# Performance work log

Hardware: AMD Instinct MI355X
Metric: run time of the kernel (lower is better)

## Reference

```python
import jax, jax.numpy as jnp
import numpy as np

B, S, P, E, H, FF = 4, 16, 256, 768, 12, 3072
HD = E // H
LN_EPS = 1e-5


def _layernorm(x, g, b):
    m = jnp.mean(x, axis=-1, keepdims=True)
    v = jnp.mean((x - m) ** 2, axis=-1, keepdims=True)
    return (x - m) * jax.lax.rsqrt(v + LN_EPS) * g + b


def _qkv(x, wqkv, bqkv):
    # wqkv: [3, E, E] (in, out layout), bqkv: [3, E]
    qkv = jnp.einsum('bspe,tef->tbspf', x, wqkv) + bqkv[:, None, None, None, :]
    q, k, v = qkv
    b, s, p, e = x.shape
    shp = (b, s, p, H, HD)
    return q.reshape(shp), k.reshape(shp), v.reshape(shp)


def spatial_attn(x, wqkv, bqkv, wo, bo, g, beta):
    q, k, v = _qkv(x, wqkv, bqkv)  # [b,s,p,n,d]
    scale = 1.0 / np.sqrt(HD).astype(np.float32)
    scores = jnp.einsum('bsind,bsjnd->bsnij', q, k) * scale  # [b,s,n,p,p]
    attn = jax.nn.softmax(scores, axis=-1)
    out = jnp.einsum('bsnij,bsjnd->bsind', attn, v)  # [b,s,p,n,d]
    out = out.reshape(x.shape)
    out = out @ wo + bo
    return _layernorm(x + out, g, beta)


def temporal_attn(x, wqkv, bqkv, wo, bo, g, beta):
    q, k, v = _qkv(x, wqkv, bqkv)  # [b,s,p,n,d]
    scale = 1.0 / np.sqrt(HD).astype(np.float32)
    scores = jnp.einsum('bipnd,bjpnd->bpnij', q, k) * scale  # [b,p,n,s,s]
    s = x.shape[1]
    causal = jnp.tril(jnp.ones((s, s), dtype=bool))
    scores = jnp.where(causal, scores, jnp.float32(-jnp.inf))
    attn = jax.nn.softmax(scores, axis=-1)
    out = jnp.einsum('bpnij,bjpnd->bipnd', attn, v)  # [b,s,p,n,d]
    out = out.reshape(x.shape)
    out = out @ wo + bo
    return _layernorm(x + out, g, beta)


def ffn(x, w1, b1, w2, b2, g, beta):
    h = jax.nn.relu(x @ w1 + b1)
    out = h @ w2 + b2
    return _layernorm(x + out, g, beta)


def setup_inputs() -> dict:
    key = jax.random.key(0)
    ks = jax.random.split(key, 16)
    w = lambda k, shp: (jax.random.normal(k, shp, dtype=jnp.float32) * 0.02)
    inp = {
        'x': jax.random.normal(ks[0], (B, S, P, E), dtype=jnp.float32),
        'sa_wqkv': w(ks[1], (3, E, E)), 'sa_bqkv': jnp.zeros((3, E), jnp.float32),
        'sa_wo': w(ks[2], (E, E)), 'sa_bo': jnp.zeros((E,), jnp.float32),
        'sa_g': jnp.ones((E,), jnp.float32), 'sa_b': jnp.zeros((E,), jnp.float32),
        'ta_wqkv': w(ks[3], (3, E, E)), 'ta_bqkv': jnp.zeros((3, E), jnp.float32),
        'ta_wo': w(ks[4], (E, E)), 'ta_bo': jnp.zeros((E,), jnp.float32),
        'ta_g': jnp.ones((E,), jnp.float32), 'ta_b': jnp.zeros((E,), jnp.float32),
        'f_w1': w(ks[5], (E, FF)), 'f_b1': jnp.zeros((FF,), jnp.float32),
        'f_w2': w(ks[6], (FF, E)), 'f_b2': jnp.zeros((E,), jnp.float32),
        'f_g': jnp.ones((E,), jnp.float32), 'f_b': jnp.zeros((E,), jnp.float32),
    }
    return inp


def reference(x, sa_wqkv, sa_bqkv, sa_wo, sa_bo, sa_g, sa_b,
              ta_wqkv, ta_bqkv, ta_wo, ta_bo, ta_g, ta_b,
              f_w1, f_b1, f_w2, f_b2, f_g, f_b):
    x = spatial_attn(x, sa_wqkv, sa_bqkv, sa_wo, sa_bo, sa_g, sa_b)
    x = temporal_attn(x, ta_wqkv, ta_bqkv, ta_wo, ta_bo, ta_g, ta_b)
    x = ffn(x, f_w1, f_b1, f_w2, f_b2, f_g, f_b)
    return x
```

## Files before the change

### kernel.cpp

```cpp
#include <hip/hip_runtime.h>
#include <hip/hip_bf16.h>
#include <math.h>

constexpr int Bc = 4, Sc = 16, Pc = 256, Ec = 768, Hc = 12, HDc = 64, FFc = 3072;
constexpr int Mrows = Bc * Sc * Pc;
constexpr size_t ME = (size_t)Mrows * Ec;

typedef __attribute__((ext_vector_type(4))) float f32x4;
typedef __attribute__((ext_vector_type(8))) short s16x8;
typedef __attribute__((ext_vector_type(4))) short s16x4;

__device__ __forceinline__ short f2bf(float f) {
  union { float f; unsigned u; } v; v.f = f;
  unsigned r = (v.u + 0x7FFFu + ((v.u >> 16) & 1u)) >> 16;
  return (short)r;
}
__device__ __forceinline__ float bf2f(short s) {
  union { unsigned u; float f; } v; v.u = ((unsigned)(unsigned short)s) << 16;
  return v.f;
}

__device__ __forceinline__ void async16(const void* g, void* l) {
  __builtin_amdgcn_global_load_lds(
      (const __attribute__((address_space(1))) unsigned int*)g,
      (__attribute__((address_space(3))) unsigned int*)l, 16, 0, 0);
}

__global__ __launch_bounds__(256)
void f2bf_kernel(const float* __restrict__ in, short* __restrict__ out, int n8)
{
  int i = blockIdx.x * 256 + threadIdx.x;
  if (i >= n8) return;
  const float4* p = reinterpret_cast<const float4*>(in + (size_t)i * 8);
  float4 a = p[0], b = p[1];
  s16x8 o = { f2bf(a.x), f2bf(a.y), f2bf(a.z), f2bf(a.w),
              f2bf(b.x), f2bf(b.y), f2bf(b.z), f2bf(b.w) };
  *reinterpret_cast<s16x8*>(out + (size_t)i * 8) = o;
}

__global__ __launch_bounds__(256)
void wtrans_kernel(const float* __restrict__ Wg, short* __restrict__ Wtg,
                   int K, int N)
{
  const int z = blockIdx.z;
  const float* W  = Wg  + (size_t)z * K * N;
  short*       Wt = Wtg + (size_t)z * N * K;
  const int n0 = blockIdx.x * 64, k0 = blockIdx.y * 64;
  const int t = threadIdx.x;
  const int n  = n0 + (t >> 2);
  const int kc = k0 + (t & 3) * 16;
  short buf[16];
#pragma unroll
  for (int i = 0; i < 16; ++i)
    buf[i] = f2bf(W[(size_t)(kc + i) * N + n]);
  *reinterpret_cast<s16x8*>(&Wt[(size_t)n * K + kc])     = *reinterpret_cast<s16x8*>(&buf[0]);
  *reinterpret_cast<s16x8*>(&Wt[(size_t)n * K + kc + 8]) = *reinterpret_cast<s16x8*>(&buf[8]);
}

#define LDFRAG(base, row, kc) \
  (*reinterpret_cast<const s16x8*>((base) + (row) * 128 + ((((kc) ^ ((row) & 7)) << 4))))

#define PH_READS(Aslot, Bslot, q, LDB) \
  do { \
    if (LDB) { \
      _Pragma("unroll") \
      for (int nj = 0; nj < 4; ++nj) { \
        bfr[nj][0] = LDFRAG((Bslot), wc * 64 + nj * 16 + l16, g); \
        bfr[nj][1] = LDFRAG((Bslot), wc * 64 + nj * 16 + l16, 4 + g); \
      } \
    } \
    _Pragma("unroll") \
    for (int mi = 0; mi < BMT; ++mi) { \
      const int arow = wr * (BMT * 64) + ((q) * BMT + mi) * 16 + l16; \
      afr[mi][0] = LDFRAG((Aslot), arow, g); \
      afr[mi][1] = LDFRAG((Aslot), arow, 4 + g); \
    } \
  } while (0)

#define PH_SYNC_MMA(q) \
  do { \
    __builtin_amdgcn_sched_barrier(0); \
    __builtin_amdgcn_s_barrier(); \
    asm volatile("s_waitcnt lgkmcnt(0)" ::: "memory"); \
    __builtin_amdgcn_sched_barrier(0); \
    __builtin_amdgcn_s_setprio(1); \
    _Pragma("unroll") \
    for (int mi = 0; mi < BMT; ++mi) \
      _Pragma("unroll") \
      for (int nj = 0; nj < 4; ++nj) { \
        acc[(q) * BMT + mi][nj] = __builtin_amdgcn_mfma_f32_16x16x32_bf16( \
            afr[mi][0], bfr[nj][0], acc[(q) * BMT + mi][nj], 0, 0, 0); \
        acc[(q) * BMT + mi][nj] = __builtin_amdgcn_mfma_f32_16x16x32_bf16( \
            afr[mi][1], bfr[nj][1], acc[(q) * BMT + mi][nj], 0, 0, 0); \
      } \
    __builtin_amdgcn_s_setprio(0); \
  } while (0)

#define PH_END \
  do { __builtin_amdgcn_s_barrier(); __builtin_amdgcn_sched_barrier(0); } while (0)

#define PH_END_VM \
  do { \
    asm volatile("s_waitcnt vmcnt(4)" ::: "memory"); \
    __builtin_amdgcn_sched_barrier(0); \
    __builtin_amdgcn_s_barrier(); \
    __builtin_amdgcn_sched_barrier(0); \
  } while (0)

template<int OUT, int BMT>
__global__ __launch_bounds__(512, 2)
void gemm256_kernel(const short* __restrict__ A, const short* __restrict__ Wt,
                    const float* __restrict__ biasg, const void* __restrict__ resv,
                    void* __restrict__ Cg, short* __restrict__ vt,
                    int M, int N, int K)
{
  constexpr int ASZ = BMT * 16384;
  __shared__ char smem[2 * (ASZ + 32768)];
  const int z = blockIdx.z;
  const short* __restrict__ Wz = Wt + (size_t)z * (size_t)N * K;
  const float* __restrict__ bz = biasg + (size_t)z * N;

  const int nwg = gridDim.x;
  const int swz = ((int)blockIdx.x & 7) * (nwg >> 3) + ((int)blockIdx.x >> 3);
  const int NT = N >> 8;
  const int bm = (swz / NT) * (BMT * 128);
  const int bn = (swz % NT) << 8;

  const int tid  = threadIdx.x;
  const int lane = tid & 63;
  const int wid  = tid >> 6;
  const int wr   = wid >> 2;
  const int wc   = wid & 3;
  const int l16  = lane & 15;
  const int g    = lane >> 4;

  char* const As0 = smem;
  char* const Bs0 = smem + ASZ;
  char* const As1 = smem + ASZ + 32768;
  char* const Bs1 = smem + 2 * ASZ + 32768;

  const int srow = lane >> 3;
  const int scol = ((lane & 7) ^ srow) * 8;
  const int ldso = wid * 1024;

  auto stageG = [&](const short* __restrict__ G, int grow0, int k0, char* ldsHalf) {
    const size_t r0 = (size_t)(grow0 + wid * 8 + srow);
    async16(G + r0 * K + (k0 + scol), ldsHalf + ldso);
    async16(G + (r0 + 64) * K + (k0 + scol), ldsHalf + 8192 + ldso);
  };

  f32x4 acc[BMT * 4][4];
  s16x8 bfr[4][2];
  s16x8 afr[BMT][2];
#pragma unroll
  for (int mi = 0; mi < BMT * 4; ++mi)
#pragma unroll
    for (int nj = 0; nj < 4; ++nj) acc[mi][nj] = f32x4{0.f, 0.f, 0.f, 0.f};

  const int ntile = K >> 6;
  const int nit   = ntile >> 1;

  stageG(A, bm, 0, As0);
  if (BMT == 2) stageG(A, bm + 128, 0, As0 + 16384);
  stageG(Wz, bn,       0,  Bs0);
  stageG(Wz, bn + 128, 0,  Bs0 + 16384);
  stageG(Wz, bn,       64, Bs1);
  stageG(Wz, bn + 128, 64, Bs1 + 16384);
  asm volatile("s_waitcnt vmcnt(4)" ::: "memory");
  __builtin_amdgcn_sched_barrier(0);
  __builtin_amdgcn_s_barrier();

  for (int j = 0; j < nit; ++j) {
    const int t1k = (2 * j + 1) << 6;
    const int t2k = (2 * j + 2) << 6;
    const int t3k = (2 * j + 3) << 6;
    const bool s2 = (2 * j + 2) < ntile;
    const bool s3 = (2 * j + 3) < ntile;

    PH_READS(As0, Bs0, 0, true);
    stageG(A, bm, t1k, As1);
    PH_SYNC_MMA(0);
    PH_END;

    PH_READS(As0, Bs0, 1, false);
    if (BMT == 2) stageG(A, bm + 128, t1k, As1 + 16384);
    PH_SYNC_MMA(1);
    PH_END;

    PH_READS(As0, Bs0, 2, false);
    if (s2) stageG(Wz, bn, t2k, Bs0);
    PH_SYNC_MMA(2);
    PH_END;

    PH_READS(As0, Bs0, 3, false);
    if (s2) stageG(Wz, bn + 128, t2k, Bs0 + 16384);
    PH_SYNC_MMA(3);
    PH_END_VM;

    PH_READS(As1, Bs1, 0, true);
    if (s2) stageG(A, bm, t2k, As0);
    PH_SYNC_MMA(0);
    PH_END;

    PH_READS(As1, Bs1, 1, false);
    if (BMT == 2) { if (s2) stageG(A, bm + 128, t2k, As0 + 16384); }
    PH_SYNC_MMA(1);
    PH_END;

    PH_READS(As1, Bs1, 2, false);
    if (s3) stageG(Wz, bn, t3k, Bs1);
    PH_SYNC_MMA(2);
    PH_END;

    PH_READS(As1, Bs1, 3, false);
    if (s3) stageG(Wz, bn + 128, t3k, Bs1 + 16384);
    PH_SYNC_MMA(3);
    PH_END_VM;
  }

  const float* resf = (const float*)resv;
  const short* resb = (const short*)resv;
  short* Cb = (short*)Cg + (size_t)z * (size_t)M * N;
  float* Cf = (float*)Cg + (size_t)z * (size_t)M * N;

#pragma unroll
  for (int mi = 0; mi < BMT * 4; ++mi) {
    const int row0 = bm + wr * (BMT * 64) + mi * 16 + g * 4;
#pragma unroll
    for (int nj = 0; nj < 4; ++nj) {
      const int col = bn + wc * 64 + nj * 16 + l16;
      if (OUT == 4 && z == 2) {
        const int bs2 = row0 >> 8, p0 = row0 & 255;
        const int h2 = col >> 6,  d2 = col & 63;
        const float bias = bz[col];
        s16x4 v = { f2bf(acc[mi][nj][0] + bias), f2bf(acc[mi][nj][1] + bias),
                    f2bf(acc[mi][nj][2] + bias), f2bf(acc[mi][nj][3] + bias) };
        *reinterpret_cast<s16x4*>(
            &vt[(((size_t)bs2 * 12 + h2) * 64 + d2) * 256 + p0]) = v;
      } else {
        const float bias = bz[col];
#pragma unroll
        for (int r = 0; r < 4; ++r) {
          float v = acc[mi][nj][r] + bias;
          size_t idx = (size_t)(row0 + r) * N + col;
          if (OUT == 2) v += resf[idx];
          if (OUT == 3) v += bf2f(resb[idx]);
          if (OUT == 1) v = fmaxf(v, 0.f);
          if (OUT == 2 || OUT == 3) Cf[idx] = v;
          else                      Cb[idx] = f2bf(v);
        }
      }
    }
  }
}

__global__ __launch_bounds__(256, 3)
void spatial_attn_kernel(const short* __restrict__ Qg, const short* __restrict__ Kg,
                         const short* __restrict__ Vt, short* __restrict__ Og)
{
  const int bs = blockIdx.x;
  const int h  = blockIdx.y;

  __shared__ short Pl[4 * 32 * 64];

  const int tid  = threadIdx.x;
  const int lane = tid & 63;
  const int wid  = tid >> 6;
  const int l16  = lane & 15;
  const int g    = lane >> 4;
  const int q0   = blockIdx.z * 128 + wid * 32;
  char* Pw = (char*)Pl + wid * 4096;

  const size_t rowbase = (size_t)(bs * 256) * 768 + h * 64;
  const size_t vbase   = ((size_t)bs * 12 + h) * 64 * 256;

  s16x8 qa[2][2];
#pragma unroll
  for (int m = 0; m < 2; ++m)
#pragma unroll
    for (int ks = 0; ks < 2; ++ks)
      qa[m][ks] = *reinterpret_cast<const s16x8*>(
          &Qg[rowbase + (size_t)(q0 + m * 16 + l16) * 768 + ks * 32 + g * 8]);

  float mrun[2][4], lrun[2][4];
  f32x4 oac[2][4];
#pragma unroll
  for (int m = 0; m < 2; ++m)
#pragma unroll
    for (int r = 0; r < 4; ++r) { mrun[m][r] = -INFINITY; lrun[m][r] = 0.f; }
#pragma unroll
  for (int m = 0; m < 2; ++m)
#pragma unroll
    for (int n = 0; n < 4; ++n) oac[m][n] = f32x4{0.f, 0.f, 0.f, 0.f};

#pragma unroll
  for (int t = 0; t < 4; ++t) {
    const int key0 = t * 64;
    f32x4 sc[2][4];
#pragma unroll
    for (int m = 0; m < 2; ++m)
#pragma unroll
      for (int n = 0; n < 4; ++n) sc[m][n] = f32x4{0.f, 0.f, 0.f, 0.f};
#pragma unroll
    for (int ks = 0; ks < 2; ++ks) {
      s16x8 kf[4];
#pragma unroll
      for (int n = 0; n < 4; ++n) {
        const int key = key0 + n * 16 + l16;
        kf[n] = *reinterpret_cast<const s16x8*>(
            &Kg[rowbase + (size_t)key * 768 + ks * 32 + g * 8]);
      }
#pragma unroll
      for (int m = 0; m < 2; ++m)
#pragma unroll
        for (int n = 0; n < 4; ++n)
          sc[m][n] = __builtin_amdgcn_mfma_f32_16x16x32_bf16(qa[m][ks], kf[n], sc[m][n], 0, 0, 0);
    }
#pragma unroll
    for (int m = 0; m < 2; ++m)
#pragma unroll
      for (int n = 0; n < 4; ++n)
#pragma unroll
        for (int r = 0; r < 4; ++r) sc[m][n][r] *= 0.125f;

#pragma unroll
    for (int m = 0; m < 2; ++m) {
#pragma unroll
      for (int r = 0; r < 4; ++r) {
        float mx = fmaxf(fmaxf(sc[m][0][r], sc[m][1][r]), fmaxf(sc[m][2][r], sc[m][3][r]));
#pragma unroll
        for (int mk = 1; mk < 16; mk <<= 1) mx = fmaxf(mx, __shfl_xor(mx, mk, 64));
        const float mnew = fmaxf(mrun[m][r], mx);
        const float corr = __expf(mrun[m][r] - mnew);
        mrun[m][r] = mnew;
        float rs = 0.f;
#pragma unroll
        for (int n = 0; n < 4; ++n) {
          float p = __expf(sc[m][n][r] - mnew);
          sc[m][n][r] = p;
          rs += p;
        }
#pragma unroll
        for (int mk = 1; mk < 16; mk <<= 1) rs += __shfl_xor(rs, mk, 64);
        lrun[m][r] = lrun[m][r] * corr + rs;
#pragma unroll
        for (int nd = 0; nd < 4; ++nd) oac[m][nd][r] *= corr;
      }
    }
#pragma unroll
    for (int m = 0; m < 2; ++m)
#pragma unroll
      for (int n = 0; n < 4; ++n)
#pragma unroll
        for (int r = 0; r < 4; ++r) {
          const int q = m * 16 + g * 4 + r;
          const int key = n * 16 + l16;
          const int byte = q * 128 + (((key >> 3) ^ (q & 7)) * 16) + (key & 7) * 2;
          *reinterpret_cast<short*>(Pw + byte) = f2bf(sc[m][n][r]);
        }
#pragma unroll
    for (int ks = 0; ks < 2; ++ks) {
      s16x8 pa[2], vf[4];
#pragma unroll
      for (int m = 0; m < 2; ++m) {
        const int q = m * 16 + l16;
        const int s = ks * 4 + g;
        pa[m] = *reinterpret_cast<const s16x8*>(Pw + q * 128 + ((s ^ (q & 7)) * 16));
      }
#pragma unroll
      for (int nd = 0; nd < 4; ++nd) {
        const int d = nd * 16 + l16;
        const int key = key0 + ks * 32 + g * 8;
        vf[nd] = *reinterpret_cast<const s16x8*>(&Vt[vbase + (size_t)d * 256 + key]);
      }
#pragma unroll
      for (int m = 0; m < 2; ++m)
#pragma unroll
        for (int nd = 0; nd < 4; ++nd)
          oac[m][nd] = __builtin_amdgcn_mfma_f32_16x16x32_bf16(pa[m], vf[nd], oac[m][nd], 0, 0, 0);
    }
  }

#pragma unroll
  for (int m = 0; m < 2; ++m)
#pragma unroll
    for (int r = 0; r < 4; ++r) {
      const float inv = 1.f / lrun[m][r];
#pragma unroll
      for (int nd = 0; nd < 4; ++nd) oac[m][nd][r] *= inv;
    }
#pragma unroll
  for (int m = 0; m < 2; ++m)
#pragma unroll
    for (int nd = 0; nd < 4; ++nd)
#pragma unroll
      for (int r = 0; r < 4; ++r) {
        const int q = m * 16 + g * 4 + r;
        const int d = nd * 16 + l16;
        const int byte = q * 128 + (((d >> 3) ^ (q & 7)) * 16) + (d & 7) * 2;
        *reinterpret_cast<short*>(Pw + byte) = f2bf(oac[m][nd][r]);
      }
#pragma unroll
  for (int it = 0; it < 4; ++it) {
    const int slot = it * 64 + lane;
    const int q = slot >> 3, sl = slot & 7;
    const int d0 = (sl ^ (q & 7)) * 8;
    s16x8 v = *reinterpret_cast<const s16x8*>(Pw + slot * 16);
    *reinterpret_cast<s16x8*>(
        &Og[rowbase + (size_t)(q0 + q) * 768 + d0]) = v;
  }
}

__global__ __launch_bounds__(192)
void temporal_attn_kernel(const short* __restrict__ Qg, const short* __restrict__ Kg,
                          const short* __restrict__ Vg, short* __restrict__ Og)
{
  const int bp = blockIdx.x;
  const int b = bp >> 8, p = bp & 255;

  __shared__ short Ks[16 * 768];
  __shared__ short Vs[16 * 768];

  const int tid = threadIdx.x;
  const size_t gbase = ((size_t)(b * 16) * 256 + p) * 768;
  constexpr int SROW = 256 * 768;

  {
    const int half = tid / 96;
    const int cc   = tid - half * 96;
    const int c    = cc & 7, hs = cc >> 3;
    const int ldso = (c * 12 + hs) * 8;
#pragma unroll
    for (int it = 0; it < 8; ++it) {
      const int s = it * 2 + half;
      const size_t ga = gbase + (size_t)s * SROW + cc * 8;
      *reinterpret_cast<s16x8*>(&Ks[s * 768 + ldso]) =
          *reinterpret_cast<const s16x8*>(&Kg[ga]);
      *reinterpret_cast<s16x8*>(&Vs[s * 768 + ldso]) =
          *reinterpret_cast<const s16x8*>(&Vg[ga]);
    }
  }
  __syncthreads();

  const int h = tid % 12, i = tid / 12;
  const float scale = 0.125f;
  const size_t qoff = gbase + (size_t)i * SROW + h * 64;

  float q[HDc];
#pragma unroll
  for (int c = 0; c < 8; ++c) {
    s16x8 v = *reinterpret_cast<const s16x8*>(&Qg[qoff + c * 8]);
#pragma unroll
    for (int e = 0; e < 8; ++e) q[c * 8 + e] = bf2f(v[e]) * scale;
  }

  float m = -INFINITY, l = 0.f;
  float o[HDc];
#pragma unroll
  for (int d = 0; d < HDc; ++d) o[d] = 0.f;

  for (int j = 0; j <= i; ++j) {
    const short* kr = &Ks[j * 768];
    float s = 0.f;
#pragma unroll
    for (int c = 0; c < 8; ++c) {
      s16x8 kv = *reinterpret_cast<const s16x8*>(kr + (c * 12 + h) * 8);
#pragma unroll
      for (int e = 0; e < 8; ++e) s += q[c * 8 + e] * bf2f(kv[e]);
    }
    float mn   = fmaxf(m, s);
    float corr = __expf(m - mn);
    float pw   = __expf(s - mn);
    l = l * corr + pw;
    const short* vr = &Vs[j * 768];
#pragma unroll
    for (int c = 0; c < 8; ++c) {
      s16x8 vv = *reinterpret_cast<const s16x8*>(vr + (c * 12 + h) * 8);
#pragma unroll
      for (int e = 0; e < 8; ++e)
        o[c * 8 + e] = fmaf(pw, bf2f(vv[e]), o[c * 8 + e] * corr);
    }
    m = mn;
  }
  const float inv = 1.f / l;
  short* op = &Og[qoff];
#pragma unroll
  for (int c = 0; c < 8; ++c) {
    s16x8 v;
#pragma unroll
    for (int e = 0; e < 8; ++e) v[e] = f2bf(o[c * 8 + e] * inv);
    *reinterpret_cast<s16x8*>(op + c * 8) = v;
  }
}

template<bool OUTBF>
__global__ __launch_bounds__(256)
void layernorm_kernel(const float* __restrict__ U, const float* __restrict__ g,
                      const float* __restrict__ be, void* __restrict__ outv)
{
  const int tid  = threadIdx.x;
  const int lane = tid & 63, w = tid >> 6;
  const size_t row = (size_t)blockIdx.x * 4 + w;
  const float* u = U + row * Ec;

  float x[12];
#pragma unroll
  for (int c = 0; c < 3; ++c) {
    float4 v = *reinterpret_cast<const float4*>(&u[c * 256 + lane * 4]);
    x[c*4+0] = v.x; x[c*4+1] = v.y; x[c*4+2] = v.z; x[c*4+3] = v.w;
  }
  float s = 0.f;
#pragma unroll
  for (int k = 0; k < 12; ++k) s += x[k];
#pragma unroll
  for (int off = 32; off > 0; off >>= 1) s += __shfl_xor(s, off, 64);
  const float mean = s * (1.f / 768.f);

  float vs = 0.f;
#pragma unroll
  for (int k = 0; k < 12; ++k) { float d = x[k] - mean; vs += d * d; }
#pragma unroll
  for (int off = 32; off > 0; off >>= 1) vs += __shfl_xor(vs, off, 64);
  const float rs = rsqrtf(vs * (1.f / 768.f) + 1e-5f);

#pragma unroll
  for (int c = 0; c < 3; ++c) {
    int idx = c * 256 + lane * 4;
    float4 gv = *reinterpret_cast<const float4*>(&g[idx]);
    float4 bv = *reinterpret_cast<const float4*>(&be[idx]);
    float r0 = (x[c*4+0] - mean) * rs * gv.x + bv.x;
    float r1 = (x[c*4+1] - mean) * rs * gv.y + bv.y;
    float r2 = (x[c*4+2] - mean) * rs * gv.z + bv.z;
    float r3 = (x[c*4+3] - mean) * rs * gv.w + bv.w;
    if (OUTBF) {
      short* op = (short*)outv + row * Ec + idx;
      s16x4 v = { f2bf(r0), f2bf(r1), f2bf(r2), f2bf(r3) };
      *reinterpret_cast<s16x4*>(op) = v;
    } else {
      float* op = (float*)outv + row * Ec + idx;
      *reinterpret_cast<float4*>(op) = make_float4(r0, r1, r2, r3);
    }
  }
}

extern "C" void kernel_launch(void* const* d_in, const int* in_sizes, int n_in,
                              void* d_out, int out_size, void* d_ws, size_t ws_size,
                              hipStream_t stream)
{
  const float* x       = (const float*)d_in[0];
  const float* sa_wqkv = (const float*)d_in[1];
  const float* sa_bqkv = (const float*)d_in[2];
  const float* sa_wo   = (const float*)d_in[3];
  const float* sa_bo   = (const float*)d_in[4];
  const float* sa_g    = (const float*)d_in[5];
  const float* sa_b    = (const float*)d_in[6];
  const float* ta_wqkv = (const float*)d_in[7];
  const float* ta_bqkv = (const float*)d_in[8];
  const float* ta_wo   = (const float*)d_in[9];
  const float* ta_bo   = (const float*)d_in[10];
  const float* ta_g    = (const float*)d_in[11];
  const float* ta_b    = (const float*)d_in[12];
  const float* f_w1    = (const float*)d_in[13];
  const float* f_b1    = (const float*)d_in[14];
  const float* f_w2    = (const float*)d_in[15];
  const float* f_b2    = (const float*)d_in[16];
  const float* f_g     = (const float*)d_in[17];
  const float* f_b     = (const float*)d_in[18];

  float* out = (float*)d_out;

  constexpr size_t EE = (size_t)Ec * Ec;
  constexpr size_t WTOT = 3*EE + EE + 3*EE + EE + 2*(size_t)Ec*FFc;
  const size_t need = 14 * ME + 2 * WTOT;
  if (ws_size < need) return;

  short* Xb  = (short*)d_ws;
  short* Qb  = Xb + ME;
  short* Kb  = Qb + ME;
  short* Vtb = Qb + 2 * ME;
  short* Hb  = Qb;
  float* U   = (float*)(Xb + 5 * ME);
  short* Wtb = (short*)(U + ME);

  short* wt_sa_qkv = Wtb;
  short* wt_sa_wo  = wt_sa_qkv + 3 * EE;
  short* wt_ta_qkv = wt_sa_wo  + EE;
  short* wt_ta_wo  = wt_ta_qkv + 3 * EE;
  short* wt_f_w1   = wt_ta_wo  + EE;
  short* wt_f_w2   = wt_f_w1   + (size_t)Ec * FFc;

  wtrans_kernel<<<dim3(12, 12, 3), 256, 0, stream>>>(sa_wqkv, wt_sa_qkv, Ec, Ec);
  wtrans_kernel<<<dim3(12, 12, 1), 256, 0, stream>>>(sa_wo,   wt_sa_wo,  Ec, Ec);
  wtrans_kernel<<<dim3(12, 12, 3), 256, 0, stream>>>(ta_wqkv, wt_ta_qkv, Ec, Ec);
  wtrans_kernel<<<dim3(12, 12, 1), 256, 0, stream>>>(ta_wo,   wt_ta_wo,  Ec, Ec);
  wtrans_kernel<<<dim3(48, 12, 1), 256, 0, stream>>>(f_w1,    wt_f_w1,   Ec, FFc);
  wtrans_kernel<<<dim3(12, 48, 1), 256, 0, stream>>>(f_w2,    wt_f_w2,   FFc, Ec);
  f2bf_kernel<<<(int)(ME / 8 / 256), 256, 0, stream>>>(x, Xb, (int)(ME / 8));

  const dim3 gQKV((Mrows / 256) * (Ec / 256), 1, 3);
  const dim3 gSQ ((Mrows / 128) * (Ec / 256), 1, 1);
  const dim3 gFF1((Mrows / 256) * (FFc / 256), 1, 1);

  gemm256_kernel<4, 2><<<gQKV, 512, 0, stream>>>(Xb, wt_sa_qkv, sa_bqkv, nullptr, Qb, Vtb, Mrows, Ec, Ec);
  spatial_attn_kernel<<<dim3(Bc * Sc, Hc, 2), 256, 0, stream>>>(Qb, Kb, Vtb, Qb);
  gemm256_kernel<2, 1><<<gSQ, 512, 0, stream>>>(Qb, wt_sa_wo, sa_bo, x, U, nullptr, Mrows, Ec, Ec);
  layernorm_kernel<true><<<Mrows / 4, 256, 0, stream>>>(U, sa_g, sa_b, Xb);

  gemm256_kernel<0, 2><<<gQKV, 512, 0, stream>>>(Xb, wt_ta_qkv, ta_bqkv, nullptr, Qb, nullptr, Mrows, Ec, Ec);
  temporal_attn_kernel<<<Bc * Pc, 192, 0, stream>>>(Qb, Kb, Vtb, Qb);
  gemm256_kernel<3, 1><<<gSQ, 512, 0, stream>>>(Qb, wt_ta_wo, ta_bo, Xb, U, nullptr, Mrows, Ec, Ec);
  layernorm_kernel<true><<<Mrows / 4, 256, 0, stream>>>(U, ta_g, ta_b, Xb);

  gemm256_kernel<1, 2><<<gFF1, 512, 0, stream>>>(Xb, wt_f_w1, f_b1, nullptr, Hb, nullptr, Mrows, FFc, Ec);
  gemm256_kernel<3, 1><<<gSQ, 512, 0, stream>>>(Hb, wt_f_w2, f_b2, Xb, U, nullptr, Mrows, Ec, FFc);
  layernorm_kernel<false><<<Mrows / 4, 256, 0, stream>>>(U, f_g, f_b, out);
}
```

Measured before the change: 613.5 us.

## Merge prep kernels into one launch and store pre-LayerNorm sums in bf16

Merges the six weight-transpose launches and the input fp32-to-bf16 conversion into one prep kernel that dispatches on block index. The GEMM epilogues that add the residual now always write bf16, and the LayerNorm kernels read bf16 instead of fp32. The first output projection takes its residual from bf16 Xb rather than fp32 x. This halves traffic on the intermediate buffer and removes launch overhead, at the cost of extra rounding before LayerNorm, including a bf16 residual in the first block.

```diff
diff --git a/kernel.cpp b/kernel.cpp
--- a/kernel.cpp
+++ b/kernel.cpp
@@ -26,27 +26,10 @@
       (__attribute__((address_space(3))) unsigned int*)l, 16, 0, 0);
 }
 
-__global__ __launch_bounds__(256)
-void f2bf_kernel(const float* __restrict__ in, short* __restrict__ out, int n8)
+__device__ __forceinline__ void wtrans_tile(const float* __restrict__ W,
+                                            short* __restrict__ Wt,
+                                            int K, int N, int n0, int k0, int t)
 {
-  int i = blockIdx.x * 256 + threadIdx.x;
-  if (i >= n8) return;
-  const float4* p = reinterpret_cast<const float4*>(in + (size_t)i * 8);
-  float4 a = p[0], b = p[1];
-  s16x8 o = { f2bf(a.x), f2bf(a.y), f2bf(a.z), f2bf(a.w),
-              f2bf(b.x), f2bf(b.y), f2bf(b.z), f2bf(b.w) };
-  *reinterpret_cast<s16x8*>(out + (size_t)i * 8) = o;
-}
-
-__global__ __launch_bounds__(256)
-void wtrans_kernel(const float* __restrict__ Wg, short* __restrict__ Wtg,
-                   int K, int N)
-{
-  const int z = blockIdx.z;
-  const float* W  = Wg  + (size_t)z * K * N;
-  short*       Wt = Wtg + (size_t)z * N * K;
-  const int n0 = blockIdx.x * 64, k0 = blockIdx.y * 64;
-  const int t = threadIdx.x;
   const int n  = n0 + (t >> 2);
   const int kc = k0 + (t & 3) * 16;
   short buf[16];
@@ -55,6 +38,49 @@
     buf[i] = f2bf(W[(size_t)(kc + i) * N + n]);
   *reinterpret_cast<s16x8*>(&Wt[(size_t)n * K + kc])     = *reinterpret_cast<s16x8*>(&buf[0]);
   *reinterpret_cast<s16x8*>(&Wt[(size_t)n * K + kc + 8]) = *reinterpret_cast<s16x8*>(&buf[8]);
+}
+
+__global__ __launch_bounds__(256)
+void prep_kernel(const float* __restrict__ x, short* __restrict__ Xb,
+                 const float* __restrict__ saqkv, short* __restrict__ wt_saqkv,
+                 const float* __restrict__ sawo,  short* __restrict__ wt_sawo,
+                 const float* __restrict__ taqkv, short* __restrict__ wt_taqkv,
+                 const float* __restrict__ tawo,  short* __restrict__ wt_tawo,
+                 const float* __restrict__ fw1,   short* __restrict__ wt_fw1,
+                 const float* __restrict__ fw2,   short* __restrict__ wt_fw2)
+{
+  const int b = blockIdx.x;
+  const int t = threadIdx.x;
+  constexpr size_t EE = (size_t)Ec * Ec;
+
+  if (b < 432) {
+    const int z = b / 144, tl = b % 144;
+    wtrans_tile(saqkv + (size_t)z * EE, wt_saqkv + (size_t)z * EE,
+                Ec, Ec, (tl % 12) * 64, (tl / 12) * 64, t);
+  } else if (b < 576) {
+    const int tl = b - 432;
+    wtrans_tile(sawo, wt_sawo, Ec, Ec, (tl % 12) * 64, (tl / 12) * 64, t);
+  } else if (b < 1008) {
+    const int z = (b - 576) / 144, tl = (b - 576) % 144;
+    wtrans_tile(taqkv + (size_t)z * EE, wt_taqkv + (size_t)z * EE,
+                Ec, Ec, (tl % 12) * 64, (tl / 12) * 64, t);
+  } else if (b < 1152) {
+    const int tl = b - 1008;
+    wtrans_tile(tawo, wt_tawo, Ec, Ec, (tl % 12) * 64, (tl / 12) * 64, t);
+  } else if (b < 1728) {
+    const int tl = b - 1152;
+    wtrans_tile(fw1, wt_fw1, Ec, FFc, (tl % 48) * 64, (tl / 48) * 64, t);
+  } else if (b < 2304) {
+    const int tl = b - 1728;
+    wtrans_tile(fw2, wt_fw2, FFc, Ec, (tl % 12) * 64, (tl / 12) * 64, t);
+  } else {
+    const size_t i = (size_t)(b - 2304) * 256 + t;
+    const float4* p = reinterpret_cast<const float4*>(x + i * 8);
+    float4 a = p[0], bb = p[1];
+    s16x8 o = { f2bf(a.x), f2bf(a.y), f2bf(a.z), f2bf(a.w),
+                f2bf(bb.x), f2bf(bb.y), f2bf(bb.z), f2bf(bb.w) };
+    *reinterpret_cast<s16x8*>(Xb + i * 8) = o;
+  }
 }
 
 #define LDFRAG(base, row, kc) \
@@ -218,10 +244,8 @@
     PH_END_VM;
   }
 
-  const float* resf = (const float*)resv;
   const short* resb = (const short*)resv;
   short* Cb = (short*)Cg + (size_t)z * (size_t)M * N;
-  float* Cf = (float*)Cg + (size_t)z * (size_t)M * N;
 
 #pragma unroll
   for (int mi = 0; mi < BMT * 4; ++mi) {
@@ -243,11 +267,9 @@
         for (int r = 0; r < 4; ++r) {
           float v = acc[mi][nj][r] + bias;
           size_t idx = (size_t)(row0 + r) * N + col;
-          if (OUT == 2) v += resf[idx];
           if (OUT == 3) v += bf2f(resb[idx]);
           if (OUT == 1) v = fmaxf(v, 0.f);
-          if (OUT == 2 || OUT == 3) Cf[idx] = v;
-          else                      Cb[idx] = f2bf(v);
+          Cb[idx] = f2bf(v);
         }
       }
     }
@@ -495,19 +517,20 @@
 
 template<bool OUTBF>
 __global__ __launch_bounds__(256)
-void layernorm_kernel(const float* __restrict__ U, const float* __restrict__ g,
+void layernorm_kernel(const short* __restrict__ U, const float* __restrict__ g,
                       const float* __restrict__ be, void* __restrict__ outv)
 {
   const int tid  = threadIdx.x;
   const int lane = tid & 63, w = tid >> 6;
   const size_t row = (size_t)blockIdx.x * 4 + w;
-  const float* u = U + row * Ec;
+  const short* u = U + row * Ec;
 
   float x[12];
 #pragma unroll
   for (int c = 0; c < 3; ++c) {
-    float4 v = *reinterpret_cast<const float4*>(&u[c * 256 + lane * 4]);
-    x[c*4+0] = v.x; x[c*4+1] = v.y; x[c*4+2] = v.z; x[c*4+3] = v.w;
+    s16x4 v = *reinterpret_cast<const s16x4*>(&u[c * 256 + lane * 4]);
+    x[c*4+0] = bf2f(v[0]); x[c*4+1] = bf2f(v[1]);
+    x[c*4+2] = bf2f(v[2]); x[c*4+3] = bf2f(v[3]);
   }
   float s = 0.f;
 #pragma unroll
@@ -571,7 +594,7 @@
 
   constexpr size_t EE = (size_t)Ec * Ec;
   constexpr size_t WTOT = 3*EE + EE + 3*EE + EE + 2*(size_t)Ec*FFc;
-  const size_t need = 14 * ME + 2 * WTOT;
+  const size_t need = 12 * ME + 2 * WTOT;
   if (ws_size < need) return;
 
   short* Xb  = (short*)d_ws;
@@ -579,8 +602,8 @@
   short* Kb  = Qb + ME;
   short* Vtb = Qb + 2 * ME;
   short* Hb  = Qb;
-  float* U   = (float*)(Xb + 5 * ME);
-  short* Wtb = (short*)(U + ME);
+  short* U   = Xb + 5 * ME;
+  short* Wtb = U + ME;
 
   short* wt_sa_qkv = Wtb;
   short* wt_sa_wo  = wt_sa_qkv + 3 * EE;
@@ -589,13 +612,9 @@
   short* wt_f_w1   = wt_ta_wo  + EE;
   short* wt_f_w2   = wt_f_w1   + (size_t)Ec * FFc;
 
-  wtrans_kernel<<<dim3(12, 12, 3), 256, 0, stream>>>(sa_wqkv, wt_sa_qkv, Ec, Ec);
-  wtrans_kernel<<<dim3(12, 12, 1), 256, 0, stream>>>(sa_wo,   wt_sa_wo,  Ec, Ec);
-  wtrans_kernel<<<dim3(12, 12, 3), 256, 0, stream>>>(ta_wqkv, wt_ta_qkv, Ec, Ec);
-  wtrans_kernel<<<dim3(12, 12, 1), 256, 0, stream>>>(ta_wo,   wt_ta_wo,  Ec, Ec);
-  wtrans_kernel<<<dim3(48, 12, 1), 256, 0, stream>>>(f_w1,    wt_f_w1,   Ec, FFc);
-  wtrans_kernel<<<dim3(12, 48, 1), 256, 0, stream>>>(f_w2,    wt_f_w2,   FFc, Ec);
-  f2bf_kernel<<<(int)(ME / 8 / 256), 256, 0, stream>>>(x, Xb, (int)(ME / 8));
+  prep_kernel<<<8448, 256, 0, stream>>>(
+      x, Xb, sa_wqkv, wt_sa_qkv, sa_wo, wt_sa_wo,
+      ta_wqkv, wt_ta_qkv, ta_wo, wt_ta_wo, f_w1, wt_f_w1, f_w2, wt_f_w2);
 
   const dim3 gQKV((Mrows / 256) * (Ec / 256), 1, 3);
   const dim3 gSQ ((Mrows / 128) * (Ec / 256), 1, 1);
@@ -603,7 +622,7 @@
 
   gemm256_kernel<4, 2><<<gQKV, 512, 0, stream>>>(Xb, wt_sa_qkv, sa_bqkv, nullptr, Qb, Vtb, Mrows, Ec, Ec);
   spatial_attn_kernel<<<dim3(Bc * Sc, Hc, 2), 256, 0, stream>>>(Qb, Kb, Vtb, Qb);
-  gemm256_kernel<2, 1><<<gSQ, 512, 0, stream>>>(Qb, wt_sa_wo, sa_bo, x, U, nullptr, Mrows, Ec, Ec);
+  gemm256_kernel<3, 1><<<gSQ, 512, 0, stream>>>(Qb, wt_sa_wo, sa_bo, Xb, U, nullptr, Mrows, Ec, Ec);
   layernorm_kernel<true><<<Mrows / 4, 256, 0, stream>>>(U, sa_g, sa_b, Xb);
 
   gemm256_kernel<0, 2><<<gQKV, 512, 0, stream>>>(Xb, wt_ta_qkv, ta_bqkv, nullptr, Qb, nullptr, Mrows, Ec, Ec);
```

New measurement: 578.1 us. -5.8%, faster.
